# Kernel optimization log

Measured on AMD Instinct MI355X. Metric: run time of the kernel, lower is better.

## Reference

```python
import jax, jax.numpy as jnp
import numpy as np

EMBED_DIM = 1024
NUM_HEADS = 16
HEAD_DIM = EMBED_DIM // NUM_HEADS


def setup_inputs() -> dict:
    key = jax.random.key(0)
    ks = jax.random.split(key, 12)
    B, S, E = 2, 2048, EMBED_DIM
    scale = 1.0 / np.sqrt(E)
    inp = {
        "query": jax.random.normal(ks[0], (B, S, E), dtype=jnp.float32),
        "key": jax.random.normal(ks[1], (B, S, E), dtype=jnp.float32),
        "value": jax.random.normal(ks[2], (B, S, E), dtype=jnp.float32),
        "key_padding_mask": jax.random.randint(ks[3], (B, S), 0, 2).astype(bool),
        # Linear params (torch nn.Linear: y = x @ W.T + b)
        "Wq": jax.random.normal(ks[4], (E, E), dtype=jnp.float32) * scale,
        "bq": jnp.zeros((E,), dtype=jnp.float32),
        "Wk": jax.random.normal(ks[5], (E, E), dtype=jnp.float32) * scale,
        "bk": jnp.zeros((E,), dtype=jnp.float32),
        "Wv": jax.random.normal(ks[6], (E, E), dtype=jnp.float32) * scale,
        "bv": jnp.zeros((E,), dtype=jnp.float32),
        "Wo": jax.random.normal(ks[7], (E, E), dtype=jnp.float32) * scale,
        "bo": jnp.zeros((E,), dtype=jnp.float32),
    }
    return inp


def reference(query, key, value, key_padding_mask, Wq, bq, Wk, bk, Wv, bv, Wo, bo):
    B, Sq, E = query.shape
    H, D = NUM_HEADS, HEAD_DIM

    def split_heads(x, W, b):
        y = x @ W.T + b                      # [B, S, E]
        return y.reshape(B, -1, H, D).transpose(0, 2, 1, 3)  # [B, H, S, D]

    q = split_heads(query, Wq, bq)
    k = split_heads(key, Wk, bk)
    v = split_heads(value, Wv, bv)

    scores = jnp.einsum("bhqd,bhkd->bhqk", q, k) / jnp.sqrt(jnp.float32(D))
    scores = jnp.where(key_padding_mask[:, None, None, :], -jnp.inf, scores)
    probs = jax.nn.softmax(scores, axis=-1)  # dropout p=0.0 -> identity
    attn = jnp.einsum("bhqk,bhkd->bhqd", probs, v)
    attn = attn.transpose(0, 2, 1, 3).reshape(B, Sq, E)
    return attn @ Wo.T + bo
```

## Files before the change

### kernel.cpp

```cpp
#include <hip/hip_runtime.h>
#include <hip/hip_bf16.h>

#define BATCH 2
#define SEQ   2048
#define EMBED 1024
#define NHEAD 16
#define HDIM  64

typedef __bf16 bf16x8 __attribute__((ext_vector_type(8)));
typedef __bf16 bf16x4 __attribute__((ext_vector_type(4)));
typedef float  floatx4 __attribute__((ext_vector_type(4)));

struct ConvAll { const void* src[7]; void* dst[7]; unsigned n[7]; };

__device__ __forceinline__ int derive_isbf(const void* qptr) {
    const unsigned short* u = (const unsigned short*)qptr;
    int sane = 0;
    for (int k = 0; k < 64; ++k) {
        int e = (u[2 * k] >> 7) & 0xff;
        if (e >= 117 && e <= 137) sane++;
    }
    return (sane >= 40) ? 1 : 0;
}

__global__ __launch_bounds__(256) void prep_convert(
        ConvAll a, const void* qptr, const void* mptr,
        int* flags, __hip_bfloat16* mones) {
    if (blockIdx.y == 7) {
        if (blockIdx.x >= 16) return;
        const unsigned int* w = (const unsigned int*)mptr;
        int all01 = 1, allf = 1;
        for (int i = 0; i < 64; ++i) {
            unsigned int x = w[i];
            if (!(x == 0u || x == 1u)) all01 = 0;
            if (!(x == 0u || x == 0x3F800000u)) allf = 0;
        }
        const int bytemask = (all01 || allf) ? 0 : 1;
        const int i = blockIdx.x * 256 + threadIdx.x;
        int v;
        if (bytemask) v = (((const unsigned char*)mptr)[i] != 0);
        else          v = (((const unsigned int*)mptr)[i] != 0u);
        mones[i] = __float2bfloat16(v ? 0.f : 1.f);
        if (blockIdx.x == 0 && threadIdx.x == 0) {
            flags[0] = derive_isbf(qptr);
            flags[1] = bytemask;
        }
        return;
    }
    if (derive_isbf(qptr)) return;
    const int t = blockIdx.y;
    const unsigned n8 = a.n[t] / 8;
    const unsigned stride = gridDim.x * blockDim.x;
    for (unsigned i = blockIdx.x * blockDim.x + threadIdx.x; i < n8; i += stride) {
        const unsigned base = i * 8;
        const float* s = (const float*)a.src[t] + base;
        __hip_bfloat16 tmp[8];
#pragma unroll
        for (int j = 0; j < 8; ++j) tmp[j] = __float2bfloat16(s[j]);
        *(uint4*)((__hip_bfloat16*)a.dst[t] + base) = *(const uint4*)tmp;
    }
}

__device__ __forceinline__ void gload_lds16(const __hip_bfloat16* g, __bf16* l) {
    __builtin_amdgcn_global_load_lds(
        (const __attribute__((address_space(1))) unsigned int*)g,
        (__attribute__((address_space(3))) unsigned int*)l, 16, 0, 0);
}

struct GemmIO {
    const void* Xr; const __hip_bfloat16* Xc;
    const void* Wr; const __hip_bfloat16* Wc;
    const void* br;
    void* Y;
    float osc;
};
struct GemmArgs { GemmIO io[3]; };

__global__ __launch_bounds__(256, 2) void gemm_mfma(
        GemmArgs args, int M, int N, int K, const int* flags,
        const __hip_bfloat16* __restrict__ mones) {
    const GemmIO io = args.io[blockIdx.z];
    const int isbf = flags[0];
    const __hip_bfloat16* Xp = isbf ? (const __hip_bfloat16*)io.Xr : io.Xc;
    const __hip_bfloat16* Wp = isbf ? (const __hip_bfloat16*)io.Wr : io.Wc;
    __shared__ __bf16 Xs[128 * 64];
    __shared__ __bf16 Ws[128 * 64];
    const int lane = threadIdx.x & 63, wv = threadIdx.x >> 6;
    const int wr = wv >> 1, wc = wv & 1;
    const int l = lane & 15, quad = lane >> 4;
    const int row0 = blockIdx.y * 128, col0 = blockIdx.x * 128;

    const int srow = lane >> 3;
    const int schunk = (lane & 7) ^ srow;
    const __hip_bfloat16* xbase = Xp + (size_t)(row0 + srow) * K + schunk * 8;
    const __hip_bfloat16* wbase = Wp + (size_t)(col0 + srow) * K + schunk * 8;

    floatx4 acc[4][4] = {};

    for (int k0 = 0; k0 < K; k0 += 64) {
        __syncthreads();
#pragma unroll
        for (int i = 0; i < 4; ++i) {
            const int instr = wv * 4 + i;
            gload_lds16(xbase + (size_t)instr * 8 * K + k0, &Xs[instr * 512]);
        }
#pragma unroll
        for (int i = 0; i < 4; ++i) {
            const int instr = wv * 4 + i;
            gload_lds16(wbase + (size_t)instr * 8 * K + k0, &Ws[instr * 512]);
        }
        __syncthreads();
#pragma unroll
        for (int kk = 0; kk < 2; ++kk) {
            bf16x8 af[4], bfr[4];
#pragma unroll
            for (int m = 0; m < 4; ++m)
                af[m] = *(const bf16x8*)
                    &Xs[(wr * 64 + m * 16 + l) * 64 + ((kk * 4 + quad) ^ (l & 7)) * 8];
#pragma unroll
            for (int n = 0; n < 4; ++n)
                bfr[n] = *(const bf16x8*)
                    &Ws[(wc * 64 + n * 16 + l) * 64 + ((kk * 4 + quad) ^ (l & 7)) * 8];
#pragma unroll
            for (int m = 0; m < 4; ++m)
#pragma unroll
                for (int n = 0; n < 4; ++n)
                    acc[m][n] = __builtin_amdgcn_mfma_f32_16x16x32_bf16(
                        af[m], bfr[n], acc[m][n], 0, 0, 0);
        }
    }

    if (blockIdx.z == 2) {
#pragma unroll
        for (int m = 0; m < 4; ++m) {
            const int rb = row0 + wr * 64 + m * 16 + quad * 4;
            const int b = rb >> 11, s0 = rb & (SEQ - 1);
            float mf[4];
#pragma unroll
            for (int r = 0; r < 4; ++r)
                mf[r] = __bfloat162float(mones[rb + r]);
#pragma unroll
            for (int n = 0; n < 4; ++n) {
                const int col = col0 + wc * 64 + n * 16 + l;
                const int h = col >> 6, d = col & 63;
                const float bv = isbf
                    ? __bfloat162float(((const __hip_bfloat16*)io.br)[col])
                    : ((const float*)io.br)[col];
                bf16x4 out;
#pragma unroll
                for (int r = 0; r < 4; ++r)
                    out[r] = (__bf16)((acc[m][n][r] + bv) * mf[r]);
                *(bf16x4*)((__hip_bfloat16*)io.Y +
                           ((size_t)((b << 4) + h) * HDIM + d) * SEQ + s0) = out;
            }
        }
    } else {
#pragma unroll
        for (int m = 0; m < 4; ++m) {
#pragma unroll
            for (int n = 0; n < 4; ++n) {
                const int col = col0 + wc * 64 + n * 16 + l;
                const float bv = isbf
                    ? __bfloat162float(((const __hip_bfloat16*)io.br)[col])
                    : ((const float*)io.br)[col];
#pragma unroll
                for (int r = 0; r < 4; ++r) {
                    const int row = row0 + wr * 64 + m * 16 + quad * 4 + r;
                    const float v = (acc[m][n][r] + bv) * io.osc;
                    ((__hip_bfloat16*)io.Y)[(size_t)row * N + col] = __float2bfloat16(v);
                }
            }
        }
    }
}

__global__ __launch_bounds__(256, 2) void gemm_out(
        const __hip_bfloat16* __restrict__ X,
        const void* __restrict__ Wr, const __hip_bfloat16* __restrict__ Wc,
        const void* __restrict__ bias, void* __restrict__ Y,
        const int* flags) {
    const int N = EMBED, K = EMBED;
    const int isbf = flags[0];
    const __hip_bfloat16* Wp = isbf ? (const __hip_bfloat16*)Wr : Wc;
    __shared__ __bf16 Xs[64 * 64];
    __shared__ __bf16 Ws[128 * 64];
    const int lane = threadIdx.x & 63, wv = threadIdx.x >> 6;
    const int wr = wv >> 1, wc = wv & 1;
    const int l = lane & 15, quad = lane >> 4;
    const int row0 = blockIdx.y * 64, col0 = blockIdx.x * 128;

    const int srow = lane >> 3;
    const int schunk = (lane & 7) ^ srow;
    const __hip_bfloat16* xbase = X + (size_t)(row0 + srow) * K + schunk * 8;
    const __hip_bfloat16* wbase = Wp + (size_t)(col0 + srow) * K + schunk * 8;

    floatx4 acc[2][4] = {};

    for (int k0 = 0; k0 < K; k0 += 64) {
        __syncthreads();
#pragma unroll
        for (int i = 0; i < 2; ++i) {
            const int instr = wv * 2 + i;
            gload_lds16(xbase + (size_t)instr * 8 * K + k0, &Xs[instr * 512]);
        }
#pragma unroll
        for (int i = 0; i < 4; ++i) {
            const int instr = wv * 4 + i;
            gload_lds16(wbase + (size_t)instr * 8 * K + k0, &Ws[instr * 512]);
        }
        __syncthreads();
#pragma unroll
        for (int kk = 0; kk < 2; ++kk) {
            bf16x8 af[2], bfr[4];
#pragma unroll
            for (int m = 0; m < 2; ++m)
                af[m] = *(const bf16x8*)
                    &Xs[(wr * 32 + m * 16 + l) * 64 + ((kk * 4 + quad) ^ (l & 7)) * 8];
#pragma unroll
            for (int n = 0; n < 4; ++n)
                bfr[n] = *(const bf16x8*)
                    &Ws[(wc * 64 + n * 16 + l) * 64 + ((kk * 4 + quad) ^ (l & 7)) * 8];
#pragma unroll
            for (int m = 0; m < 2; ++m)
#pragma unroll
                for (int n = 0; n < 4; ++n)
                    acc[m][n] = __builtin_amdgcn_mfma_f32_16x16x32_bf16(
                        af[m], bfr[n], acc[m][n], 0, 0, 0);
        }
    }

#pragma unroll
    for (int m = 0; m < 2; ++m) {
#pragma unroll
        for (int n = 0; n < 4; ++n) {
            const int col = col0 + wc * 64 + n * 16 + l;
            const float bv = isbf
                ? __bfloat162float(((const __hip_bfloat16*)bias)[col])
                : ((const float*)bias)[col];
#pragma unroll
            for (int r = 0; r < 4; ++r) {
                const int row = row0 + wr * 32 + m * 16 + quad * 4 + r;
                const float v = acc[m][n][r] + bv;
                if (isbf)
                    ((__hip_bfloat16*)Y)[(size_t)row * N + col] = __float2bfloat16(v);
                else
                    ((float*)Y)[(size_t)row * N + col] = v;
            }
        }
    }
}

__global__ __launch_bounds__(256) void attn_mfma(
        const __hip_bfloat16* __restrict__ Qb,
        const __hip_bfloat16* __restrict__ Kb,
        const __hip_bfloat16* __restrict__ Vt,
        const __hip_bfloat16* __restrict__ mones,
        __hip_bfloat16* __restrict__ Ao) {
    const int bh = blockIdx.x, b = bh >> 4, h = bh & 15;
    const int q0 = blockIdx.y * 128;
    const int wv = threadIdx.x >> 6, lane = threadIdx.x & 63;
    const int l = lane & 15, quad = lane >> 4;

    __shared__ __bf16 Ks[2][128 * 64];
    __shared__ __bf16 Vs[2][64 * 128];

    bf16x8 aQ[2][2];
#pragma unroll
    for (int g = 0; g < 2; ++g) {
        const int qrow = q0 + wv * 32 + g * 16 + l;
        const __hip_bfloat16* qp =
            Qb + ((size_t)(b * SEQ + qrow)) * EMBED + h * HDIM + quad * 8;
        aQ[g][0] = *(const bf16x8*)qp;
        aQ[g][1] = *(const bf16x8*)(qp + 32);
    }

    floatx4 O[2][4] = {};
    floatx4 Ol[2] = {};
    const int rho = 8 * (l >> 2) + (l & 3);

    const int ksrow = lane >> 3, kpc = lane & 7;
    const int vsrow = lane >> 4, vpc = lane & 15;
    const __hip_bfloat16* mbase = mones + b * SEQ;

    auto stage = [&](int k0, int buf) {
#pragma unroll
        for (int i = 0; i < 4; ++i) {
            const int row = wv * 32 + i * 8 + ksrow;
            const int sc = kpc ^ ((row & 3) | (((row >> 3) & 1) << 2));
            gload_lds16(Kb + ((size_t)(b * SEQ + k0 + row)) * EMBED + h * HDIM +
                            sc * 8,
                        &Ks[buf][(wv * 32 + i * 8) * 64]);
        }
#pragma unroll
        for (int i = 0; i < 4; ++i) {
            const int row = wv * 16 + i * 4 + vsrow;
            const int sc = vpc ^ (row & 15);
            gload_lds16(Vt + ((size_t)(bh * HDIM + row)) * SEQ + k0 + sc * 8,
                        &Vs[buf][(wv * 16 + i * 4) * 128]);
        }
    };

    auto compute = [&](int k0, int buf) {
#pragma unroll
        for (int kh2 = 0; kh2 < 2; ++kh2) {
            bf16x8 a0[4], a1[4];
#pragma unroll
            for (int n = 0; n < 4; ++n) {
                const int rr = kh2 * 64 + 32 * (n >> 1) + 4 * (n & 1) + rho;
                const int f = (rr & 3) | (((rr >> 3) & 1) << 2);
                a0[n] = *(const bf16x8*)&Ks[buf][rr * 64 + ((quad) ^ f) * 8];
                a1[n] = *(const bf16x8*)&Ks[buf][rr * 64 + ((quad + 4) ^ f) * 8];
            }
            bf16x8 bv[2][4];
#pragma unroll
            for (int kh = 0; kh < 2; ++kh)
#pragma unroll
                for (int dt = 0; dt < 4; ++dt) {
                    const int c = kh2 * 8 + kh * 4 + quad;
                    bv[kh][dt] = *(const bf16x8*)
                        &Vs[buf][(dt * 16 + l) * 128 + (c ^ l) * 8];
                }
            bf16x8 vm[2];
#pragma unroll
            for (int kh = 0; kh < 2; ++kh)
                vm[kh] = *(const bf16x8*)
                    (mbase + k0 + kh2 * 64 + kh * 32 + quad * 8);

#pragma unroll
            for (int g = 0; g < 2; ++g) {
                floatx4 S[4];
                __builtin_amdgcn_s_setprio(1);
#pragma unroll
                for (int n = 0; n < 4; ++n) {
                    floatx4 c = {};
                    c = __builtin_amdgcn_mfma_f32_16x16x32_bf16(a0[n], aQ[g][0],
                                                                c, 0, 0, 0);
                    c = __builtin_amdgcn_mfma_f32_16x16x32_bf16(a1[n], aQ[g][1],
                                                                c, 0, 0, 0);
                    S[n] = c;
                }
                __builtin_amdgcn_s_setprio(0);
#pragma unroll
                for (int n = 0; n < 4; ++n)
#pragma unroll
                    for (int r = 0; r < 4; ++r)
                        S[n][r] = __builtin_amdgcn_exp2f(S[n][r]);
#pragma unroll
                for (int kh = 0; kh < 2; ++kh) {
                    bf16x8 ap;
#pragma unroll
                    for (int j = 0; j < 4; ++j) {
                        ap[j]     = (__bf16)S[2 * kh][j];
                        ap[j + 4] = (__bf16)S[2 * kh + 1][j];
                    }
                    __builtin_amdgcn_s_setprio(1);
#pragma unroll
                    for (int dt = 0; dt < 4; ++dt)
                        O[g][dt] = __builtin_amdgcn_mfma_f32_16x16x32_bf16(
                            ap, bv[kh][dt], O[g][dt], 0, 0, 0);
                    Ol[g] = __builtin_amdgcn_mfma_f32_16x16x32_bf16(
                        ap, vm[kh], Ol[g], 0, 0, 0);
                    __builtin_amdgcn_s_setprio(0);
                }
            }
        }
    };

    stage(0, 0);
    const int NT = SEQ / 128;
    for (int tt = 0; tt < NT; tt += 2) {
        __syncthreads();
        stage((tt + 1) * 128, 1);
        compute(tt * 128, 0);
        __syncthreads();
        if (tt + 2 < NT) stage((tt + 2) * 128, 0);
        compute((tt + 1) * 128, 1);
    }
#pragma unroll
    for (int g = 0; g < 2; ++g)
#pragma unroll
        for (int r = 0; r < 4; ++r) {
            const float lr = Ol[g][r];
            const float inv = (lr > 0.f) ? __builtin_amdgcn_rcpf(lr) : 0.f;
            const int row = q0 + wv * 32 + g * 16 + quad * 4 + r;
#pragma unroll
            for (int dt = 0; dt < 4; ++dt)
                Ao[((size_t)(b * SEQ + row)) * EMBED + h * HDIM + dt * 16 + l] =
                    __float2bfloat16(O[g][dt][r] * inv);
        }
}

extern "C" void kernel_launch(void* const* d_in, const int* in_sizes, int n_in,
                              void* d_out, int out_size, void* d_ws, size_t ws_size,
                              hipStream_t stream) {
    const void* query = d_in[0];
    const void* key   = d_in[1];
    const void* value = d_in[2];
    const void* mask  = d_in[3];

    char* ws = (char*)d_ws;
    int* flags = (int*)ws;
    __hip_bfloat16* mones = (__hip_bfloat16*)(ws + 2048);
    const size_t TEN = (size_t)BATCH * SEQ * EMBED;
    const size_t WEL = (size_t)EMBED * EMBED;
    char* p = ws + 32768;
    __hip_bfloat16* Qc  = (__hip_bfloat16*)p;  p += TEN * 2;
    __hip_bfloat16* Kc  = (__hip_bfloat16*)p;  p += TEN * 2;
    __hip_bfloat16* Vc  = (__hip_bfloat16*)p;  p += TEN * 2;
    __hip_bfloat16* Wqc = (__hip_bfloat16*)p;  p += WEL * 2;
    __hip_bfloat16* Wkc = (__hip_bfloat16*)p;  p += WEL * 2;
    __hip_bfloat16* Wvc = (__hip_bfloat16*)p;  p += WEL * 2;
    __hip_bfloat16* Woc = (__hip_bfloat16*)p;  p += WEL * 2;
    __hip_bfloat16* Qb  = (__hip_bfloat16*)p;  p += TEN * 2;
    __hip_bfloat16* Kb  = (__hip_bfloat16*)p;  p += TEN * 2;
    __hip_bfloat16* Vt  = (__hip_bfloat16*)p;  p += TEN * 2;
    __hip_bfloat16* Ao  = Qc;

    const int M = BATCH * SEQ;
    const float QSCALE = 0.125f * 1.44269504088896f;

    ConvAll ca;
    ca.src[0] = query;    ca.dst[0] = Qc;  ca.n[0] = (unsigned)TEN;
    ca.src[1] = key;      ca.dst[1] = Kc;  ca.n[1] = (unsigned)TEN;
    ca.src[2] = value;    ca.dst[2] = Vc;  ca.n[2] = (unsigned)TEN;
    ca.src[3] = d_in[4];  ca.dst[3] = Wqc; ca.n[3] = (unsigned)WEL;
    ca.src[4] = d_in[6];  ca.dst[4] = Wkc; ca.n[4] = (unsigned)WEL;
    ca.src[5] = d_in[8];  ca.dst[5] = Wvc; ca.n[5] = (unsigned)WEL;
    ca.src[6] = d_in[10]; ca.dst[6] = Woc; ca.n[6] = (unsigned)WEL;
    prep_convert<<<dim3(256, 8), 256, 0, stream>>>(ca, query, mask, flags, mones);

    GemmArgs qkv;
    qkv.io[0] = { query, Qc, d_in[4],  Wqc, d_in[5],  (void*)Qb, QSCALE };
    qkv.io[1] = { key,   Kc, d_in[6],  Wkc, d_in[7],  (void*)Kb, 1.0f };
    qkv.io[2] = { value, Vc, d_in[8],  Wvc, d_in[9],  (void*)Vt, 1.0f };
    gemm_mfma<<<dim3(EMBED / 128, M / 128, 3), 256, 0, stream>>>(
        qkv, M, EMBED, EMBED, flags, mones);

    attn_mfma<<<dim3(BATCH * NHEAD, SEQ / 128), 256, 0, stream>>>(
        Qb, Kb, Vt, mones, Ao);

    gemm_out<<<dim3(EMBED / 128, M / 64), 256, 0, stream>>>(
        Ao, d_in[10], Woc, d_in[11], d_out, flags);
}
```

Before: 226.4 us.

## Double-buffer LDS tiles in QKV and output projection GEMMs

Result: slower. 233.0 us (+2.9%).

```diff
diff --git a/kernel.cpp b/kernel.cpp
--- a/kernel.cpp
+++ b/kernel.cpp
@@ -83,8 +83,8 @@
     const int isbf = flags[0];
     const __hip_bfloat16* Xp = isbf ? (const __hip_bfloat16*)io.Xr : io.Xc;
     const __hip_bfloat16* Wp = isbf ? (const __hip_bfloat16*)io.Wr : io.Wc;
-    __shared__ __bf16 Xs[128 * 64];
-    __shared__ __bf16 Ws[128 * 64];
+    __shared__ __bf16 Xs[2][128 * 64];
+    __shared__ __bf16 Ws[2][128 * 64];
     const int lane = threadIdx.x & 63, wv = threadIdx.x >> 6;
     const int wr = wv >> 1, wc = wv & 1;
     const int l = lane & 15, quad = lane >> 4;
@@ -97,30 +97,31 @@
 
     floatx4 acc[4][4] = {};
 
-    for (int k0 = 0; k0 < K; k0 += 64) {
-        __syncthreads();
+    auto stage = [&](int k0, int buf) {
 #pragma unroll
         for (int i = 0; i < 4; ++i) {
             const int instr = wv * 4 + i;
-            gload_lds16(xbase + (size_t)instr * 8 * K + k0, &Xs[instr * 512]);
+            gload_lds16(xbase + (size_t)instr * 8 * K + k0, &Xs[buf][instr * 512]);
         }
 #pragma unroll
         for (int i = 0; i < 4; ++i) {
             const int instr = wv * 4 + i;
-            gload_lds16(wbase + (size_t)instr * 8 * K + k0, &Ws[instr * 512]);
-        }
-        __syncthreads();
+            gload_lds16(wbase + (size_t)instr * 8 * K + k0, &Ws[buf][instr * 512]);
+        }
+    };
+
+    auto compute = [&](int buf) {
 #pragma unroll
         for (int kk = 0; kk < 2; ++kk) {
             bf16x8 af[4], bfr[4];
 #pragma unroll
             for (int m = 0; m < 4; ++m)
                 af[m] = *(const bf16x8*)
-                    &Xs[(wr * 64 + m * 16 + l) * 64 + ((kk * 4 + quad) ^ (l & 7)) * 8];
+                    &Xs[buf][(wr * 64 + m * 16 + l) * 64 + ((kk * 4 + quad) ^ (l & 7)) * 8];
 #pragma unroll
             for (int n = 0; n < 4; ++n)
                 bfr[n] = *(const bf16x8*)
-                    &Ws[(wc * 64 + n * 16 + l) * 64 + ((kk * 4 + quad) ^ (l & 7)) * 8];
+                    &Ws[buf][(wc * 64 + n * 16 + l) * 64 + ((kk * 4 + quad) ^ (l & 7)) * 8];
 #pragma unroll
             for (int m = 0; m < 4; ++m)
 #pragma unroll
@@ -128,6 +129,16 @@
                     acc[m][n] = __builtin_amdgcn_mfma_f32_16x16x32_bf16(
                         af[m], bfr[n], acc[m][n], 0, 0, 0);
         }
+    };
+
+    stage(0, 0);
+    for (int k0 = 0; k0 < K; k0 += 128) {
+        __syncthreads();
+        if (k0 + 64 < K) stage(k0 + 64, 1);
+        compute(0);
+        __syncthreads();
+        if (k0 + 128 < K) stage(k0 + 128, 0);
+        compute(1);
     }
 
     if (blockIdx.z == 2) {
@@ -182,8 +193,8 @@
     const int N = EMBED, K = EMBED;
     const int isbf = flags[0];
     const __hip_bfloat16* Wp = isbf ? (const __hip_bfloat16*)Wr : Wc;
-    __shared__ __bf16 Xs[64 * 64];
-    __shared__ __bf16 Ws[128 * 64];
+    __shared__ __bf16 Xs[2][64 * 64];
+    __shared__ __bf16 Ws[2][128 * 64];
     const int lane = threadIdx.x & 63, wv = threadIdx.x >> 6;
     const int wr = wv >> 1, wc = wv & 1;
     const int l = lane & 15, quad = lane >> 4;
@@ -196,30 +207,31 @@
 
     floatx4 acc[2][4] = {};
 
-    for (int k0 = 0; k0 < K; k0 += 64) {
-        __syncthreads();
+    auto stage = [&](int k0, int buf) {
 #pragma unroll
         for (int i = 0; i < 2; ++i) {
             const int instr = wv * 2 + i;
-            gload_lds16(xbase + (size_t)instr * 8 * K + k0, &Xs[instr * 512]);
+            gload_lds16(xbase + (size_t)instr * 8 * K + k0, &Xs[buf][instr * 512]);
         }
 #pragma unroll
         for (int i = 0; i < 4; ++i) {
             const int instr = wv * 4 + i;
-            gload_lds16(wbase + (size_t)instr * 8 * K + k0, &Ws[instr * 512]);
-        }
-        __syncthreads();
+            gload_lds16(wbase + (size_t)instr * 8 * K + k0, &Ws[buf][instr * 512]);
+        }
+    };
+
+    auto compute = [&](int buf) {
 #pragma unroll
         for (int kk = 0; kk < 2; ++kk) {
             bf16x8 af[2], bfr[4];
 #pragma unroll
             for (int m = 0; m < 2; ++m)
                 af[m] = *(const bf16x8*)
-                    &Xs[(wr * 32 + m * 16 + l) * 64 + ((kk * 4 + quad) ^ (l & 7)) * 8];
+                    &Xs[buf][(wr * 32 + m * 16 + l) * 64 + ((kk * 4 + quad) ^ (l & 7)) * 8];
 #pragma unroll
             for (int n = 0; n < 4; ++n)
                 bfr[n] = *(const bf16x8*)
-                    &Ws[(wc * 64 + n * 16 + l) * 64 + ((kk * 4 + quad) ^ (l & 7)) * 8];
+                    &Ws[buf][(wc * 64 + n * 16 + l) * 64 + ((kk * 4 + quad) ^ (l & 7)) * 8];
 #pragma unroll
             for (int m = 0; m < 2; ++m)
 #pragma unroll
@@ -227,6 +239,16 @@
                     acc[m][n] = __builtin_amdgcn_mfma_f32_16x16x32_bf16(
                         af[m], bfr[n], acc[m][n], 0, 0, 0);
         }
+    };
+
+    stage(0, 0);
+    for (int k0 = 0; k0 < K; k0 += 128) {
+        __syncthreads();
+        if (k0 + 64 < K) stage(k0 + 64, 1);
+        compute(0);
+        __syncthreads();
+        if (k0 + 128 < K) stage(k0 + 128, 0);
+        compute(1);
     }
 
 #pragma unroll
```
